# Kernel optimization log

Measured on AMD Instinct MI355X. Metric: run time of the kernel, lower is better.

Reference implementation:

```python
import jax, jax.numpy as jnp
import numpy as np

NUM_CLUSTERS = 64
NUM_ITERS = 3
TEMPERATURE = 0.1
CENTER_EMA = 0.99


def _l2norm(x, eps=1e-12):
    n = jnp.linalg.norm(x, axis=-1, keepdims=True)
    return x / jnp.maximum(n, eps)


def setup_inputs() -> dict:
    key = jax.random.key(0)
    k1, k2 = jax.random.split(key)
    B, N, d = 16, 4096, 768
    features = jax.random.normal(k1, (B, N, d), dtype=jnp.float32)
    centers = jax.random.normal(k2, (NUM_CLUSTERS, d), dtype=jnp.float32)
    return {"features": features, "centers": centers}


def reference(features, centers):
    B, N, d = features.shape
    K = centers.shape[0]
    M = B * N  # single-device: M_total == M_local

    features_norm = _l2norm(features)          # [B, N, d]
    centers_n = _l2norm(centers)               # [K, d]

    logits = jnp.einsum('bnd,kd->bnk', features_norm, centers_n) / TEMPERATURE
    Q = jnp.exp(logits.astype(jnp.float32).reshape(M, K).T)  # [K, M]

    Q = Q / jnp.maximum(Q.sum(), 1e-12)
    for _ in range(NUM_ITERS):
        row_sums = Q.sum(axis=1, keepdims=True)              # [K, 1]
        Q = Q / (jnp.maximum(row_sums, 1e-12) * float(K))
        col_sums = Q.sum(axis=0, keepdims=True)              # [1, M]
        Q = Q / (jnp.maximum(col_sums, 1e-12) * float(M))

    assignments = (Q * float(M)).T.reshape(B, N, K).astype(features.dtype)

    # EMA center update
    Q_flat = assignments.reshape(M, K)
    feat_flat = features_norm.reshape(M, d)
    weighted = jnp.einsum('mk,md->kd', Q_flat, feat_flat)    # [K, d]
    mass = Q_flat.sum(axis=0)                                # [K]
    new_centers = _l2norm(weighted / jnp.maximum(mass, 1e-6)[:, None])
    updated = CENTER_EMA * centers_n + (1.0 - CENTER_EMA) * new_centers
    updated = _l2norm(updated)

    return assignments, updated
```

## Files before the change

kernel.cpp:

```cpp
#include <hip/hip_runtime.h>
#include <hip/hip_bf16.h>

#define M_TOTAL 65536
#define DIM 768
#define KC 64
#define INV_T 10.0f

#define DT 128
#define MB 64
#define CH 8
#define MSEG 128

#define LOGITS_BLOCKS (M_TOTAL / 64)
#define SROWS 128
#define SINK_BLOCKS (M_TOTAL / SROWS)

typedef __attribute__((ext_vector_type(4))) float f32x4;
typedef __attribute__((ext_vector_type(8))) short bf16x8;
typedef __attribute__((ext_vector_type(4))) unsigned short u16x4;

__device__ __forceinline__ short f2bf(float f) {
    __hip_bfloat16 h = __float2bfloat16(f);
    union { __hip_bfloat16 h; short s; } u; u.h = h;
    return u.s;
}

__global__ __launch_bounds__(256) void k_centers(const float* __restrict__ centers,
                                                 float* __restrict__ cn,
                                                 short* __restrict__ cnbf) {
    int k = blockIdx.x, tid = threadIdx.x;
    float ss = 0.f;
    for (int i = tid; i < DIM; i += 256) { float v = centers[k * DIM + i]; ss += v * v; }
    __shared__ float red[4];
    for (int o = 32; o; o >>= 1) ss += __shfl_xor(ss, o);
    if ((tid & 63) == 0) red[tid >> 6] = ss;
    __syncthreads();
    ss = red[0] + red[1] + red[2] + red[3];
    float inv = 1.0f / fmaxf(sqrtf(ss), 1e-12f);
    for (int i = tid; i < DIM; i += 256) {
        float v = centers[k * DIM + i] * inv;
        cn[k * DIM + i] = v;
        cnbf[k * DIM + i] = f2bf(v);
    }
}

__global__ __launch_bounds__(256) void k_logits(const float* __restrict__ F,
                                                const short* __restrict__ cnbf,
                                                float* __restrict__ E,
                                                float* __restrict__ invn,
                                                float* __restrict__ PS0) {
    __shared__ float fbuf[2][4096];
    __shared__ float bsr[4][KC];
    int tid = threadIdx.x;
    int wave = tid >> 6, lane = tid & 63;
    int l15 = lane & 15, lhi = lane >> 4;
    int rowbase = blockIdx.x * 64;

    int srow = tid >> 4;
    int c4 = (tid & 15) * 4;

    f32x4 acc[4];
#pragma unroll
    for (int n = 0; n < 4; ++n) acc[n] = (f32x4){0.f, 0.f, 0.f, 0.f};
    float ss = 0.f;

    auto stage = [&](int t, int b) {
#pragma unroll
        for (int i = 0; i < 4; ++i) {
            int row = i * 16 + srow;
            const float* src = F + (size_t)(rowbase + row) * DIM + t * 64 + (c4 ^ ((row & 7) << 2));
            float* dst = &fbuf[b][i * 1024 + wave * 256];
            __builtin_amdgcn_global_load_lds((const __attribute__((address_space(1))) void*)src,
                                             (__attribute__((address_space(3))) void*)dst, 16, 0, 0);
        }
    };

    stage(0, 0);
    __syncthreads();

    int myrow = wave * 16 + l15;
    int swz = (l15 & 7) << 2;
    const short* Bb = cnbf + (size_t)l15 * DIM + lhi * 8;

    for (int t = 0; t < 12; ++t) {
        int cur = t & 1;
        if (t < 11) stage(t + 1, cur ^ 1);
        const float* cb = fbuf[cur] + myrow * 64;
#pragma unroll
        for (int kk = 0; kk < 64; kk += 32) {
            int c0s = (kk + lhi * 8) ^ swz;
            f32x4 fa = *(const f32x4*)(cb + c0s);
            f32x4 fb2 = *(const f32x4*)(cb + (c0s ^ 4));
            ss += fa[0] * fa[0] + fa[1] * fa[1] + fa[2] * fa[2] + fa[3] * fa[3]
                + fb2[0] * fb2[0] + fb2[1] * fb2[1] + fb2[2] * fb2[2] + fb2[3] * fb2[3];
            bf16x8 af;
            af[0] = f2bf(fa[0]); af[1] = f2bf(fa[1]); af[2] = f2bf(fa[2]); af[3] = f2bf(fa[3]);
            af[4] = f2bf(fb2[0]); af[5] = f2bf(fb2[1]); af[6] = f2bf(fb2[2]); af[7] = f2bf(fb2[3]);
#pragma unroll
            for (int n = 0; n < 4; ++n) {
                bf16x8 b = *(const bf16x8*)(Bb + (size_t)n * 16 * DIM + t * 64 + kk);
                acc[n] = __builtin_amdgcn_mfma_f32_16x16x32_bf16(af, b, acc[n], 0, 0, 0);
            }
        }
        __syncthreads();
    }

    ss += __shfl_xor(ss, 16);
    ss += __shfl_xor(ss, 32);
    float inv = 1.0f / fmaxf(sqrtf(ss), 1e-12f);
    int growbase = rowbase + wave * 16;
    if (lane < 16) invn[growbase + lane] = inv;

    float sc[4];
#pragma unroll
    for (int j = 0; j < 4; ++j) sc[j] = __shfl(inv, lhi * 4 + j) * INV_T;

    float colp[4] = {0.f, 0.f, 0.f, 0.f};
#pragma unroll
    for (int n = 0; n < 4; ++n) {
#pragma unroll
        for (int j = 0; j < 4; ++j) {
            float e = expf(acc[n][j] * sc[j]);
            int row = lhi * 4 + j;
            E[(size_t)(growbase + row) * KC + ((n * 16 + l15) ^ (row << 2))] = e;
            colp[n] += e;
        }
    }
#pragma unroll
    for (int n = 0; n < 4; ++n) {
        colp[n] += __shfl_xor(colp[n], 16);
        colp[n] += __shfl_xor(colp[n], 32);
    }
    if (lane < 16) {
#pragma unroll
        for (int n = 0; n < 4; ++n) bsr[wave][n * 16 + lane] = colp[n];
    }
    __syncthreads();
    if (tid < KC) PS0[(size_t)blockIdx.x * KC + tid] =
        bsr[0][tid] + bsr[1][tid] + bsr[2][tid] + bsr[3][tid];
}

template <int STAGE>
__global__ __launch_bounds__(1024) void k_redR(const float* __restrict__ PS, int nblocks,
                                               const float* __restrict__ Rin,
                                               float* __restrict__ Rout) {
    __shared__ float part[16][KC];
    int k = threadIdx.x & 63, g = threadIdx.x >> 6;
    float s = 0.f;
    for (int p = g; p < nblocks; p += 16) s += PS[(size_t)p * KC + k];
    part[g][k] = s;
    __syncthreads();
    if (threadIdx.x < KC) {
        float sk = 0.f;
#pragma unroll
        for (int g2 = 0; g2 < 16; ++g2) sk += part[g2][k];
        if (STAGE == 0) {
            float tot = sk;
            for (int o = 32; o; o >>= 1) tot += __shfl_xor(tot, o);
            float S = fmaxf(tot, 1e-12f);
            Rout[k] = (1.0f / S) / (fmaxf(sk / S, 1e-12f) * 64.0f);
        } else {
            float r = Rin[k];
            Rout[k] = r / (fmaxf(r * sk, 1e-12f) * 64.0f);
        }
    }
}

template <int MODE>
__global__ __launch_bounds__(256) void k_sink(const float* __restrict__ E,
                                              const float* __restrict__ R,
                                              const float* __restrict__ invn,
                                              float* __restrict__ c,
                                              float* __restrict__ PS,
                                              float* __restrict__ Aout,
                                              short* __restrict__ Qbf) {
    __shared__ float tile[SROWS * KC];
    __shared__ float sbuf[SROWS];
    __shared__ float Rlds[KC];
    __shared__ float bacc[4][KC];
    int tid = threadIdx.x, lane = tid & 63, wave = tid >> 6;
    int m0 = blockIdx.x * SROWS;

    if (tid < KC) Rlds[tid] = R[tid];

#pragma unroll
    for (int i = 0; i < 8; ++i) {
        const float* src = E + (size_t)(m0 + i * 16 + wave * 4 + (lane >> 4)) * KC + (lane & 15) * 4;
        float* dst = tile + (i * 16 + wave * 4) * KC;
        __builtin_amdgcn_global_load_lds((const __attribute__((address_space(1))) void*)src,
                                         (__attribute__((address_space(3))) void*)dst, 16, 0, 0);
    }
    __syncthreads();

#pragma unroll
    for (int i = 0; i < 32; ++i) {
        int idx = tid + i * 256;
        int mloc = idx >> 6, ccol = idx & 63;
        tile[idx] *= Rlds[ccol ^ ((mloc & 15) << 2)];
    }
    __syncthreads();

    if (tid < SROWS) {
        const float* rp = tile + tid * KC;
        int sw = tid & 15;
        f32x4 a0 = {0.f, 0.f, 0.f, 0.f}, a1 = {0.f, 0.f, 0.f, 0.f};
#pragma unroll
        for (int j = 0; j < 16; j += 2) {
            a0 += *(const f32x4*)(rp + ((j ^ sw) << 2));
            a1 += *(const f32x4*)(rp + (((j + 1) ^ sw) << 2));
        }
        f32x4 a = a0 + a1;
        sbuf[tid] = a[0] + a[1] + a[2] + a[3];
    }
    __syncthreads();

    float wacc = 0.f;
    int rbase = wave * 32;
#pragma unroll 4
    for (int r = 0; r < 32; ++r) {
        int rr = rbase + r;
        int m = m0 + rr;
        float v = tile[rr * KC + (lane ^ ((rr & 15) << 2))];
        float s = sbuf[rr];
        float cold = (MODE == 0) ? 1.0f : c[m];
        float cnew = cold / (fmaxf(cold * s, 1e-12f) * 65536.0f);
        if (MODE == 2) {
            float a = v * cnew * 65536.0f;
            size_t idx = (size_t)m * KC + lane;
            Aout[idx] = a;
            Qbf[idx] = f2bf(a * invn[m]);
            wacc += a;
        } else {
            if (lane == 0) c[m] = cnew;
            wacc += v * cnew;
        }
    }
    bacc[wave][lane] = wacc;
    __syncthreads();
    if (tid < KC) {
        float ps = bacc[0][tid] + bacc[1][tid] + bacc[2][tid] + bacc[3][tid];
        if (MODE != 2) ps /= Rlds[tid];
        PS[(size_t)blockIdx.x * KC + tid] = ps;
    }
}

__global__ __launch_bounds__(256) void k_weighted(const float* __restrict__ F,
                                                  const short* __restrict__ Qbf,
                                                  float* __restrict__ P) {
    __shared__ short ldsF[DT * MB];
    __shared__ short ldsQ[KC * MB];
    int tid = threadIdx.x;
    int dt = blockIdx.x;
    int ms = blockIdx.y;
    int wave = tid >> 6, lane = tid & 63;
    int l15 = lane & 15, lhi = lane >> 4;

    int m0 = ms * (MB * CH);
    int d0 = dt * DT;

    f32x4 acc[4][2];
#pragma unroll
    for (int kt = 0; kt < 4; ++kt)
#pragma unroll
        for (int ds = 0; ds < 2; ++ds) acc[kt][ds] = (f32x4){0.f, 0.f, 0.f, 0.f};

    int f_dq = (tid & 31) * 4;
    int f_m8 = (tid >> 5) * 8;
    int q_kq = (tid & 15) * 4;
    int q_m8 = ((tid >> 4) & 7) * 8;

    float4 rf[8];
    u16x4 q[8];
#define LOADCH(mb_)                                                                       \
    do {                                                                                  \
        _Pragma("unroll") for (int j = 0; j < 8; ++j)                                     \
            rf[j] = *(const float4*)(F + (size_t)((mb_) + f_m8 + j) * DIM + d0 + f_dq);   \
        if (tid < 128) {                                                                  \
            _Pragma("unroll") for (int j = 0; j < 8; ++j)                                 \
                q[j] = *(const u16x4*)(Qbf + (size_t)((mb_) + q_m8 + j) * KC + q_kq);     \
        }                                                                                 \
    } while (0)

    LOADCH(m0);
    for (int ch = 0; ch < CH; ++ch) {
        __syncthreads();
#pragma unroll
        for (int i = 0; i < 4; ++i) {
            int d = f_dq + i;
            uint4 w;
            w.x = (unsigned)(unsigned short)f2bf(rf[0][i]) | ((unsigned)(unsigned short)f2bf(rf[1][i]) << 16);
            w.y = (unsigned)(unsigned short)f2bf(rf[2][i]) | ((unsigned)(unsigned short)f2bf(rf[3][i]) << 16);
            w.z = (unsigned)(unsigned short)f2bf(rf[4][i]) | ((unsigned)(unsigned short)f2bf(rf[5][i]) << 16);
            w.w = (unsigned)(unsigned short)f2bf(rf[6][i]) | ((unsigned)(unsigned short)f2bf(rf[7][i]) << 16);
            int byte = (d * (MB * 2) + f_m8 * 2) ^ ((d & 7) << 4);
            *(uint4*)((char*)ldsF + byte) = w;
        }
        if (tid < 128) {
#pragma unroll
            for (int i = 0; i < 4; ++i) {
                int k = q_kq + i;
                uint4 w;
                w.x = (unsigned)q[0][i] | ((unsigned)q[1][i] << 16);
                w.y = (unsigned)q[2][i] | ((unsigned)q[3][i] << 16);
                w.z = (unsigned)q[4][i] | ((unsigned)q[5][i] << 16);
                w.w = (unsigned)q[6][i] | ((unsigned)q[7][i] << 16);
                int byte = (k * (MB * 2) + q_m8 * 2) ^ ((k & 7) << 4);
                *(uint4*)((char*)ldsQ + byte) = w;
            }
        }
        __syncthreads();
        if (ch + 1 < CH) LOADCH(m0 + (ch + 1) * MB);
#pragma unroll
        for (int h = 0; h < 2; ++h) {
            bf16x8 afr[4];
#pragma unroll
            for (int kt = 0; kt < 4; ++kt) {
                int k = kt * 16 + l15;
                int byte = (k * (MB * 2) + (h * 32 + lhi * 8) * 2) ^ ((k & 7) << 4);
                afr[kt] = *(bf16x8*)((char*)ldsQ + byte);
            }
#pragma unroll
            for (int ds = 0; ds < 2; ++ds) {
                int d = wave * 32 + ds * 16 + l15;
                int byte = (d * (MB * 2) + (h * 32 + lhi * 8) * 2) ^ ((d & 7) << 4);
                bf16x8 bfr = *(bf16x8*)((char*)ldsF + byte);
#pragma unroll
                for (int kt = 0; kt < 4; ++kt)
                    acc[kt][ds] = __builtin_amdgcn_mfma_f32_16x16x32_bf16(afr[kt], bfr, acc[kt][ds], 0, 0, 0);
            }
        }
    }
#undef LOADCH

    float* Pb = P + (size_t)ms * (KC * DIM) + d0;
#pragma unroll
    for (int kt = 0; kt < 4; ++kt)
#pragma unroll
        for (int ds = 0; ds < 2; ++ds) {
            int d = wave * 32 + ds * 16 + l15;
#pragma unroll
            for (int r4 = 0; r4 < 4; ++r4) {
                int k = kt * 16 + lhi * 4 + r4;
                Pb[(size_t)k * DIM + d] = acc[kt][ds][r4];
            }
        }
}

__global__ __launch_bounds__(128) void k_reducep(const float* __restrict__ P,
                                                 float* __restrict__ W) {
    int o = blockIdx.x * 128 + threadIdx.x;
    const float* p = P + o;
    float s0 = 0.f, s1 = 0.f, s2 = 0.f, s3 = 0.f;
    size_t stride = (size_t)KC * DIM;
#pragma unroll 4
    for (int g = 0; g < MSEG; g += 4) {
        s0 += p[(size_t)g * stride];
        s1 += p[(size_t)(g + 1) * stride];
        s2 += p[(size_t)(g + 2) * stride];
        s3 += p[(size_t)(g + 3) * stride];
    }
    W[o] = (s0 + s1) + (s2 + s3);
}

__global__ __launch_bounds__(256) void k_final(const float* __restrict__ W,
                                               const float* __restrict__ PSM,
                                               const float* __restrict__ cn,
                                               float* __restrict__ outC) {
    int k = blockIdx.x, tid = threadIdx.x;
    __shared__ float red[4];

    float msum = 0.f;
    for (int p = tid; p < SINK_BLOCKS; p += 256) msum += PSM[(size_t)p * KC + k];
    for (int o = 32; o; o >>= 1) msum += __shfl_xor(msum, o);
    if ((tid & 63) == 0) red[tid >> 6] = msum;
    __syncthreads();
    float mk = fmaxf(red[0] + red[1] + red[2] + red[3], 1e-6f);
    __syncthreads();

    float w[3];
#pragma unroll
    for (int g = 0; g < 3; ++g) w[g] = W[k * DIM + tid + g * 256] / mk;

    float ss = w[0] * w[0] + w[1] * w[1] + w[2] * w[2];
    for (int o = 32; o; o >>= 1) ss += __shfl_xor(ss, o);
    if ((tid & 63) == 0) red[tid >> 6] = ss;
    __syncthreads();
    ss = red[0] + red[1] + red[2] + red[3];
    float n1 = fmaxf(sqrtf(ss), 1e-12f);
    __syncthreads();

    float u0 = 0.99f * cn[k * DIM + tid]       + 0.01f * (w[0] / n1);
    float u1 = 0.99f * cn[k * DIM + tid + 256] + 0.01f * (w[1] / n1);
    float u2 = 0.99f * cn[k * DIM + tid + 512] + 0.01f * (w[2] / n1);
    float ss2 = u0 * u0 + u1 * u1 + u2 * u2;
    for (int o = 32; o; o >>= 1) ss2 += __shfl_xor(ss2, o);
    if ((tid & 63) == 0) red[tid >> 6] = ss2;
    __syncthreads();
    ss2 = red[0] + red[1] + red[2] + red[3];
    float n2 = fmaxf(sqrtf(ss2), 1e-12f);

    outC[k * DIM + tid]       = u0 / n2;
    outC[k * DIM + tid + 256] = u1 / n2;
    outC[k * DIM + tid + 512] = u2 / n2;
}

extern "C" void kernel_launch(void* const* d_in, const int* in_sizes, int n_in,
                              void* d_out, int out_size, void* d_ws, size_t ws_size,
                              hipStream_t stream) {
    const float* F = (const float*)d_in[0];
    const float* centers = (const float*)d_in[1];
    float* out = (float*)d_out;
    float* A = out;
    float* outC = out + (size_t)M_TOTAL * KC;

    float* w = (float*)d_ws;
    float* cn   = w;
    short* cnbf = (short*)(w + 49152);
    float* R0   = w + 73728;
    float* R1   = w + 73792;
    float* R2   = w + 73856;
    float* invn = w + 74048;
    float* cbuf = w + 139584;
    float* E    = w + 205120;
    short* Qbf  = (short*)(w + 4399424);
    float* PS0  = w + 6496576;
    float* PS1  = w + 6562112;
    float* PS2  = w + 6594880;
    float* PSM  = w + 6627648;
    float* partial = w + 6660416;
    float* weighted = w + 12951872;

    k_centers<<<KC, 256, 0, stream>>>(centers, cn, cnbf);
    k_logits<<<LOGITS_BLOCKS, 256, 0, stream>>>(F, cnbf, E, invn, PS0);
    k_redR<0><<<1, 1024, 0, stream>>>(PS0, LOGITS_BLOCKS, nullptr, R0);
    k_sink<0><<<SINK_BLOCKS, 256, 0, stream>>>(E, R0, invn, cbuf, PS1, A, Qbf);
    k_redR<1><<<1, 1024, 0, stream>>>(PS1, SINK_BLOCKS, R0, R1);
    k_sink<1><<<SINK_BLOCKS, 256, 0, stream>>>(E, R1, invn, cbuf, PS2, A, Qbf);
    k_redR<1><<<1, 1024, 0, stream>>>(PS2, SINK_BLOCKS, R1, R2);
    k_sink<2><<<SINK_BLOCKS, 256, 0, stream>>>(E, R2, invn, cbuf, PSM, A, Qbf);

    dim3 wgrid(DIM / DT, MSEG);
    k_weighted<<<wgrid, 256, 0, stream>>>(F, Qbf, partial);
    k_reducep<<<(KC * DIM) / 128, 128, 0, stream>>>(partial, weighted);
    k_final<<<KC, 256, 0, stream>>>(weighted, PSM, cn, outC);
}
```

Before: 193.8 us.

## Triple-buffer logits staging with register B prefetch; fold partial reduction into final

The logits kernel moves from a double-buffered to a triple-buffered LDS pipeline. It uses explicit vmcnt waits and raw barriers, prefetches the bf16 center fragments for the next tile into registers, and fully unrolls the tile loop. Separately, the k_reducep kernel is removed and its sum over the partial weighted buffers is done inside k_final, which saves one launch. The cost is that only 64 blocks now do the whole 128-segment reduction, and the larger LDS footprint and register pressure may lower occupancy.

```diff
diff --git a/kernel.cpp b/kernel.cpp
--- a/kernel.cpp
+++ b/kernel.cpp
@@ -49,7 +49,7 @@
                                                 float* __restrict__ E,
                                                 float* __restrict__ invn,
                                                 float* __restrict__ PS0) {
-    __shared__ float fbuf[2][4096];
+    __shared__ float fbuf[3][4096];
     __shared__ float bsr[4][KC];
     int tid = threadIdx.x;
     int wave = tid >> 6, lane = tid & 63;
@@ -59,36 +59,54 @@
     int srow = tid >> 4;
     int c4 = (tid & 15) * 4;
 
+#define STAGE(t_, b_)                                                                     \
+    do {                                                                                  \
+        _Pragma("unroll") for (int i_ = 0; i_ < 4; ++i_) {                                \
+            int row_ = i_ * 16 + srow;                                                    \
+            const float* src_ = F + (size_t)(rowbase + row_) * DIM + (t_) * 64            \
+                                + (c4 ^ ((row_ & 7) << 2));                               \
+            float* dst_ = &fbuf[b_][i_ * 1024 + wave * 256];                              \
+            __builtin_amdgcn_global_load_lds(                                             \
+                (const __attribute__((address_space(1))) void*)src_,                      \
+                (__attribute__((address_space(3))) void*)dst_, 16, 0, 0);                 \
+        }                                                                                 \
+    } while (0)
+
+    const short* Bb = cnbf + (size_t)l15 * DIM + lhi * 8;
+#define BLOAD(t_, br_)                                                                    \
+    do {                                                                                  \
+        _Pragma("unroll") for (int n_ = 0; n_ < 4; ++n_) {                                \
+            br_[n_ * 2]     = *(const bf16x8*)(Bb + (size_t)n_ * 16 * DIM + (t_) * 64);   \
+            br_[n_ * 2 + 1] = *(const bf16x8*)(Bb + (size_t)n_ * 16 * DIM + (t_) * 64 + 32); \
+        }                                                                                 \
+    } while (0)
+
+    bf16x8 bA[8], bB[8];
+    BLOAD(0, bA);
+    STAGE(0, 0);
+    STAGE(1, 1);
+
     f32x4 acc[4];
 #pragma unroll
     for (int n = 0; n < 4; ++n) acc[n] = (f32x4){0.f, 0.f, 0.f, 0.f};
     float ss = 0.f;
 
-    auto stage = [&](int t, int b) {
-#pragma unroll
-        for (int i = 0; i < 4; ++i) {
-            int row = i * 16 + srow;
-            const float* src = F + (size_t)(rowbase + row) * DIM + t * 64 + (c4 ^ ((row & 7) << 2));
-            float* dst = &fbuf[b][i * 1024 + wave * 256];
-            __builtin_amdgcn_global_load_lds((const __attribute__((address_space(1))) void*)src,
-                                             (__attribute__((address_space(3))) void*)dst, 16, 0, 0);
-        }
-    };
-
-    stage(0, 0);
-    __syncthreads();
-
     int myrow = wave * 16 + l15;
     int swz = (l15 & 7) << 2;
-    const short* Bb = cnbf + (size_t)l15 * DIM + lhi * 8;
-
+
+#pragma unroll
     for (int t = 0; t < 12; ++t) {
-        int cur = t & 1;
-        if (t < 11) stage(t + 1, cur ^ 1);
-        const float* cb = fbuf[cur] + myrow * 64;
-#pragma unroll
-        for (int kk = 0; kk < 64; kk += 32) {
-            int c0s = (kk + lhi * 8) ^ swz;
+        asm volatile("s_waitcnt vmcnt(4)" ::: "memory");
+        __builtin_amdgcn_s_barrier();
+        __builtin_amdgcn_sched_barrier(0);
+        bf16x8* bc = (t & 1) ? bB : bA;
+        bf16x8* bn = (t & 1) ? bA : bB;
+        if (t + 1 < 12) BLOAD(t + 1, bn);
+        if (t + 2 < 12) STAGE(t + 2, (t + 2) % 3);
+        const float* cb = fbuf[t % 3] + myrow * 64;
+#pragma unroll
+        for (int kk = 0; kk < 2; ++kk) {
+            int c0s = (kk * 32 + lhi * 8) ^ swz;
             f32x4 fa = *(const f32x4*)(cb + c0s);
             f32x4 fb2 = *(const f32x4*)(cb + (c0s ^ 4));
             ss += fa[0] * fa[0] + fa[1] * fa[1] + fa[2] * fa[2] + fa[3] * fa[3]
@@ -97,13 +115,12 @@
             af[0] = f2bf(fa[0]); af[1] = f2bf(fa[1]); af[2] = f2bf(fa[2]); af[3] = f2bf(fa[3]);
             af[4] = f2bf(fb2[0]); af[5] = f2bf(fb2[1]); af[6] = f2bf(fb2[2]); af[7] = f2bf(fb2[3]);
 #pragma unroll
-            for (int n = 0; n < 4; ++n) {
-                bf16x8 b = *(const bf16x8*)(Bb + (size_t)n * 16 * DIM + t * 64 + kk);
-                acc[n] = __builtin_amdgcn_mfma_f32_16x16x32_bf16(af, b, acc[n], 0, 0, 0);
-            }
-        }
-        __syncthreads();
-    }
+            for (int n = 0; n < 4; ++n)
+                acc[n] = __builtin_amdgcn_mfma_f32_16x16x32_bf16(af, bc[n * 2 + kk], acc[n], 0, 0, 0);
+        }
+    }
+#undef STAGE
+#undef BLOAD
 
     ss += __shfl_xor(ss, 16);
     ss += __shfl_xor(ss, 32);
@@ -131,6 +148,7 @@
         colp[n] += __shfl_xor(colp[n], 16);
         colp[n] += __shfl_xor(colp[n], 32);
     }
+    __syncthreads();
     if (lane < 16) {
 #pragma unroll
         for (int n = 0; n < 4; ++n) bsr[wave][n * 16 + lane] = colp[n];
@@ -346,23 +364,7 @@
         }
 }
 
-__global__ __launch_bounds__(128) void k_reducep(const float* __restrict__ P,
-                                                 float* __restrict__ W) {
-    int o = blockIdx.x * 128 + threadIdx.x;
-    const float* p = P + o;
-    float s0 = 0.f, s1 = 0.f, s2 = 0.f, s3 = 0.f;
-    size_t stride = (size_t)KC * DIM;
-#pragma unroll 4
-    for (int g = 0; g < MSEG; g += 4) {
-        s0 += p[(size_t)g * stride];
-        s1 += p[(size_t)(g + 1) * stride];
-        s2 += p[(size_t)(g + 2) * stride];
-        s3 += p[(size_t)(g + 3) * stride];
-    }
-    W[o] = (s0 + s1) + (s2 + s3);
-}
-
-__global__ __launch_bounds__(256) void k_final(const float* __restrict__ W,
+__global__ __launch_bounds__(256) void k_final(const float* __restrict__ P,
                                                const float* __restrict__ PSM,
                                                const float* __restrict__ cn,
                                                float* __restrict__ outC) {
@@ -379,7 +381,20 @@
 
     float w[3];
 #pragma unroll
-    for (int g = 0; g < 3; ++g) w[g] = W[k * DIM + tid + g * 256] / mk;
+    for (int g = 0; g < 3; ++g) {
+        int d = tid + g * 256;
+        const float* pp = P + (size_t)k * DIM + d;
+        float s0 = 0.f, s1 = 0.f, s2 = 0.f, s3 = 0.f;
+        size_t stride = (size_t)KC * DIM;
+#pragma unroll 4
+        for (int msg = 0; msg < MSEG; msg += 4) {
+            s0 += pp[(size_t)msg * stride];
+            s1 += pp[(size_t)(msg + 1) * stride];
+            s2 += pp[(size_t)(msg + 2) * stride];
+            s3 += pp[(size_t)(msg + 3) * stride];
+        }
+        w[g] = ((s0 + s1) + (s2 + s3)) / mk;
+    }
 
     float ss = w[0] * w[0] + w[1] * w[1] + w[2] * w[2];
     for (int o = 32; o; o >>= 1) ss += __shfl_xor(ss, o);
@@ -428,7 +443,6 @@
     float* PS2  = w + 6594880;
     float* PSM  = w + 6627648;
     float* partial = w + 6660416;
-    float* weighted = w + 12951872;
 
     k_centers<<<KC, 256, 0, stream>>>(centers, cn, cnbf);
     k_logits<<<LOGITS_BLOCKS, 256, 0, stream>>>(F, cnbf, E, invn, PS0);
@@ -441,6 +455,5 @@
 
     dim3 wgrid(DIM / DT, MSEG);
     k_weighted<<<wgrid, 256, 0, stream>>>(F, Qbf, partial);
-    k_reducep<<<(KC * DIM) / 128, 128, 0, stream>>>(partial, weighted);
-    k_final<<<KC, 256, 0, stream>>>(weighted, PSM, cn, outC);
-}
+    k_final<<<KC, 256, 0, stream>>>(partial, PSM, cn, outC);
+}
```

Result: slower. 199.9 us (+3.2%).

## Fold row-factor reductions into sink kernels and partial-sum reduce into final

Applied to the files above, without the earlier changes.

Removes the three single-block k_redR launches by having every k_sink block redundantly reduce the previous stage's per-block partial sums to compute the row scaling factors itself. The tile is no longer rescaled in place; the row factor is applied on the fly in the row-sum and the output write. The k_reducep launch is also removed, with k_final summing the 128 partial segments directly. This cuts four launches and their serial gaps, but every sink block now rereads the full partial-sum array, and k_final's reduction runs on only 64 blocks.

```diff
diff --git a/kernel.cpp b/kernel.cpp
--- a/kernel.cpp
+++ b/kernel.cpp
@@ -140,38 +140,14 @@
         bsr[0][tid] + bsr[1][tid] + bsr[2][tid] + bsr[3][tid];
 }
 
-template <int STAGE>
-__global__ __launch_bounds__(1024) void k_redR(const float* __restrict__ PS, int nblocks,
-                                               const float* __restrict__ Rin,
-                                               float* __restrict__ Rout) {
-    __shared__ float part[16][KC];
-    int k = threadIdx.x & 63, g = threadIdx.x >> 6;
-    float s = 0.f;
-    for (int p = g; p < nblocks; p += 16) s += PS[(size_t)p * KC + k];
-    part[g][k] = s;
-    __syncthreads();
-    if (threadIdx.x < KC) {
-        float sk = 0.f;
-#pragma unroll
-        for (int g2 = 0; g2 < 16; ++g2) sk += part[g2][k];
-        if (STAGE == 0) {
-            float tot = sk;
-            for (int o = 32; o; o >>= 1) tot += __shfl_xor(tot, o);
-            float S = fmaxf(tot, 1e-12f);
-            Rout[k] = (1.0f / S) / (fmaxf(sk / S, 1e-12f) * 64.0f);
-        } else {
-            float r = Rin[k];
-            Rout[k] = r / (fmaxf(r * sk, 1e-12f) * 64.0f);
-        }
-    }
-}
-
 template <int MODE>
 __global__ __launch_bounds__(256) void k_sink(const float* __restrict__ E,
-                                              const float* __restrict__ R,
+                                              const float* __restrict__ Rprev,
+                                              const float* __restrict__ PSprev,
                                               const float* __restrict__ invn,
                                               float* __restrict__ c,
                                               float* __restrict__ PS,
+                                              float* __restrict__ Rout,
                                               float* __restrict__ Aout,
                                               short* __restrict__ Qbf) {
     __shared__ float tile[SROWS * KC];
@@ -181,8 +157,6 @@
     int tid = threadIdx.x, lane = tid & 63, wave = tid >> 6;
     int m0 = blockIdx.x * SROWS;
 
-    if (tid < KC) Rlds[tid] = R[tid];
-
 #pragma unroll
     for (int i = 0; i < 8; ++i) {
         const float* src = E + (size_t)(m0 + i * 16 + wave * 4 + (lane >> 4)) * KC + (lane & 15) * 4;
@@ -190,58 +164,71 @@
         __builtin_amdgcn_global_load_lds((const __attribute__((address_space(1))) void*)src,
                                          (__attribute__((address_space(3))) void*)dst, 16, 0, 0);
     }
-    __syncthreads();
-
-#pragma unroll
-    for (int i = 0; i < 32; ++i) {
-        int idx = tid + i * 256;
-        int mloc = idx >> 6, ccol = idx & 63;
-        tile[idx] *= Rlds[ccol ^ ((mloc & 15) << 2)];
+
+    {
+        constexpr int NB = (MODE == 0) ? LOGITS_BLOCKS : SINK_BLOCKS;
+        int k = tid & 63, g = tid >> 6;
+        float s = 0.f;
+#pragma unroll 8
+        for (int p = g; p < NB; p += 4) s += PSprev[(size_t)p * KC + k];
+        bacc[g][k] = s;
+        __syncthreads();
+        if (tid < KC) {
+            float sk = bacc[0][k] + bacc[1][k] + bacc[2][k] + bacc[3][k];
+            float r;
+            if (MODE == 0) {
+                float tot = sk;
+                for (int o = 32; o; o >>= 1) tot += __shfl_xor(tot, o);
+                float S = fmaxf(tot, 1e-12f);
+                r = (1.0f / S) / (fmaxf(sk / S, 1e-12f) * 64.0f);
+            } else {
+                float rp = Rprev[k];
+                r = rp / (fmaxf(rp * sk, 1e-12f) * 64.0f);
+            }
+            Rlds[k] = r;
+            if (MODE != 2) Rout[k] = r;
+        }
     }
     __syncthreads();
 
     if (tid < SROWS) {
         const float* rp = tile + tid * KC;
+        const f32x4* R4 = (const f32x4*)Rlds;
         int sw = tid & 15;
-        f32x4 a0 = {0.f, 0.f, 0.f, 0.f}, a1 = {0.f, 0.f, 0.f, 0.f};
-#pragma unroll
-        for (int j = 0; j < 16; j += 2) {
-            a0 += *(const f32x4*)(rp + ((j ^ sw) << 2));
-            a1 += *(const f32x4*)(rp + (((j + 1) ^ sw) << 2));
-        }
-        f32x4 a = a0 + a1;
+        f32x4 a = {0.f, 0.f, 0.f, 0.f};
+#pragma unroll
+        for (int j = 0; j < 16; ++j)
+            a += *(const f32x4*)(rp + ((j ^ sw) << 2)) * R4[j];
         sbuf[tid] = a[0] + a[1] + a[2] + a[3];
     }
     __syncthreads();
 
+    float Rl = Rlds[lane];
     float wacc = 0.f;
     int rbase = wave * 32;
 #pragma unroll 4
     for (int r = 0; r < 32; ++r) {
         int rr = rbase + r;
         int m = m0 + rr;
-        float v = tile[rr * KC + (lane ^ ((rr & 15) << 2))];
+        float e = tile[rr * KC + (lane ^ ((rr & 15) << 2))];
         float s = sbuf[rr];
         float cold = (MODE == 0) ? 1.0f : c[m];
         float cnew = cold / (fmaxf(cold * s, 1e-12f) * 65536.0f);
         if (MODE == 2) {
-            float a = v * cnew * 65536.0f;
+            float a = e * Rl * cnew * 65536.0f;
             size_t idx = (size_t)m * KC + lane;
             Aout[idx] = a;
             Qbf[idx] = f2bf(a * invn[m]);
             wacc += a;
         } else {
             if (lane == 0) c[m] = cnew;
-            wacc += v * cnew;
+            wacc += e * cnew;
         }
     }
     bacc[wave][lane] = wacc;
     __syncthreads();
-    if (tid < KC) {
-        float ps = bacc[0][tid] + bacc[1][tid] + bacc[2][tid] + bacc[3][tid];
-        if (MODE != 2) ps /= Rlds[tid];
-        PS[(size_t)blockIdx.x * KC + tid] = ps;
-    }
+    if (tid < KC) PS[(size_t)blockIdx.x * KC + tid] =
+        bacc[0][tid] + bacc[1][tid] + bacc[2][tid] + bacc[3][tid];
 }
 
 __global__ __launch_bounds__(256) void k_weighted(const float* __restrict__ F,
@@ -346,23 +333,7 @@
         }
 }
 
-__global__ __launch_bounds__(128) void k_reducep(const float* __restrict__ P,
-                                                 float* __restrict__ W) {
-    int o = blockIdx.x * 128 + threadIdx.x;
-    const float* p = P + o;
-    float s0 = 0.f, s1 = 0.f, s2 = 0.f, s3 = 0.f;
-    size_t stride = (size_t)KC * DIM;
-#pragma unroll 4
-    for (int g = 0; g < MSEG; g += 4) {
-        s0 += p[(size_t)g * stride];
-        s1 += p[(size_t)(g + 1) * stride];
-        s2 += p[(size_t)(g + 2) * stride];
-        s3 += p[(size_t)(g + 3) * stride];
-    }
-    W[o] = (s0 + s1) + (s2 + s3);
-}
-
-__global__ __launch_bounds__(256) void k_final(const float* __restrict__ W,
+__global__ __launch_bounds__(256) void k_final(const float* __restrict__ P,
                                                const float* __restrict__ PSM,
                                                const float* __restrict__ cn,
                                                float* __restrict__ outC) {
@@ -379,7 +350,20 @@
 
     float w[3];
 #pragma unroll
-    for (int g = 0; g < 3; ++g) w[g] = W[k * DIM + tid + g * 256] / mk;
+    for (int g = 0; g < 3; ++g) {
+        int d = tid + g * 256;
+        const float* pp = P + (size_t)k * DIM + d;
+        float s0 = 0.f, s1 = 0.f, s2 = 0.f, s3 = 0.f;
+        size_t stride = (size_t)KC * DIM;
+#pragma unroll 4
+        for (int msg = 0; msg < MSEG; msg += 4) {
+            s0 += pp[(size_t)msg * stride];
+            s1 += pp[(size_t)(msg + 1) * stride];
+            s2 += pp[(size_t)(msg + 2) * stride];
+            s3 += pp[(size_t)(msg + 3) * stride];
+        }
+        w[g] = ((s0 + s1) + (s2 + s3)) / mk;
+    }
 
     float ss = w[0] * w[0] + w[1] * w[1] + w[2] * w[2];
     for (int o = 32; o; o >>= 1) ss += __shfl_xor(ss, o);
@@ -418,7 +402,6 @@
     short* cnbf = (short*)(w + 49152);
     float* R0   = w + 73728;
     float* R1   = w + 73792;
-    float* R2   = w + 73856;
     float* invn = w + 74048;
     float* cbuf = w + 139584;
     float* E    = w + 205120;
@@ -428,19 +411,14 @@
     float* PS2  = w + 6594880;
     float* PSM  = w + 6627648;
     float* partial = w + 6660416;
-    float* weighted = w + 12951872;
 
     k_centers<<<KC, 256, 0, stream>>>(centers, cn, cnbf);
     k_logits<<<LOGITS_BLOCKS, 256, 0, stream>>>(F, cnbf, E, invn, PS0);
-    k_redR<0><<<1, 1024, 0, stream>>>(PS0, LOGITS_BLOCKS, nullptr, R0);
-    k_sink<0><<<SINK_BLOCKS, 256, 0, stream>>>(E, R0, invn, cbuf, PS1, A, Qbf);
-    k_redR<1><<<1, 1024, 0, stream>>>(PS1, SINK_BLOCKS, R0, R1);
-    k_sink<1><<<SINK_BLOCKS, 256, 0, stream>>>(E, R1, invn, cbuf, PS2, A, Qbf);
-    k_redR<1><<<1, 1024, 0, stream>>>(PS2, SINK_BLOCKS, R1, R2);
-    k_sink<2><<<SINK_BLOCKS, 256, 0, stream>>>(E, R2, invn, cbuf, PSM, A, Qbf);
+    k_sink<0><<<SINK_BLOCKS, 256, 0, stream>>>(E, nullptr, PS0, invn, cbuf, PS1, R0, A, Qbf);
+    k_sink<1><<<SINK_BLOCKS, 256, 0, stream>>>(E, R0, PS1, invn, cbuf, PS2, R1, A, Qbf);
+    k_sink<2><<<SINK_BLOCKS, 256, 0, stream>>>(E, R1, PS2, invn, cbuf, PSM, nullptr, A, Qbf);
 
     dim3 wgrid(DIM / DT, MSEG);
     k_weighted<<<wgrid, 256, 0, stream>>>(F, Qbf, partial);
-    k_reducep<<<(KC * DIM) / 128, 128, 0, stream>>>(partial, weighted);
-    k_final<<<KC, 256, 0, stream>>>(weighted, PSM, cn, outC);
-}
+    k_final<<<KC, 256, 0, stream>>>(partial, PSM, cn, outC);
+}
```

After: 192.9 us. Within noise of the previous version (-0.4%).
